# Optimization experiments

Measured on AMD Instinct MI355X. Metric: run time of the kernel, lower is better.

The kernel has to match this reference:

```python
import jax, jax.numpy as jnp
import numpy as np

IN_F = 4096
OUT_F = 4096
RANK = 8
ALPHA = 8
SCALE = ALPHA / RANK


def setup_inputs() -> dict:
    key = jax.random.key(0)
    kx, kw, kb, ka = jax.random.split(key, 4)
    x = jax.random.normal(kx, (4, 4096, IN_F), dtype=jnp.float32)
    # base frozen linear params (torch Linear default init style, any values ok)
    W = jax.random.normal(kw, (OUT_F, IN_F), dtype=jnp.float32) * (1.0 / np.sqrt(IN_F))
    b = jax.random.normal(kb, (OUT_F,), dtype=jnp.float32) * 0.01
    # lora_A: kaiming_uniform_(a=sqrt(5)) -> U(-bound, bound), bound = sqrt(6/((1+5)*in_f)) = 1/sqrt(in_f)
    bound = 1.0 / np.sqrt(IN_F)
    lora_A = jax.random.uniform(ka, (RANK, IN_F), dtype=jnp.float32, minval=-bound, maxval=bound)
    # lora_B initialized to zeros per module; use small random values so the LoRA path is exercised
    lora_B = jax.random.normal(jax.random.fold_in(key, 7), (OUT_F, RANK), dtype=jnp.float32) * 0.02
    return {"x": x, "W": W, "b": b, "lora_A": lora_A, "lora_B": lora_B}


def reference(x, W, b, lora_A, lora_B):
    # base: x @ W.T + b  [B,S,out_f]
    base = jnp.einsum("bsi,oi->bso", x, W) + b
    # low-rank path: (x @ A.T) @ B.T * scale
    xa = jnp.einsum("bsi,ri->bsr", x, lora_A)  # [B,S,r]
    lora = jnp.einsum("bsr,or->bso", xa, lora_B)
    return base + lora * SCALE
```

## Files before the change

### kernel.cpp

```cpp
#include <hip/hip_runtime.h>
#include <cstdint>

#define K_IN   4096
#define N_OUT  4096
#define M_ROWS 16384
#define RANK   8
#define LSCALE 1.0f
#define NT     64

typedef __attribute__((ext_vector_type(8))) short  short8;
typedef __attribute__((ext_vector_type(4))) float  floatx4;

__device__ __forceinline__ unsigned short f2bf(float f) {
  uint32_t u = __float_as_uint(f);
  u += 0x7FFFu + ((u >> 16) & 1u);
  return (unsigned short)(u >> 16);
}

__global__ __launch_bounds__(256) void fold_w_kernel(
    const float* __restrict__ W, const float* __restrict__ lA,
    const float* __restrict__ lB, unsigned short* __restrict__ Weff) {
  int idx = blockIdx.x * 256 + threadIdx.x;
  int o = idx >> 10;
  int k = (idx & 1023) << 2;
  float4 w = *reinterpret_cast<const float4*>(W + (size_t)o * K_IN + k);
#pragma unroll
  for (int r = 0; r < RANK; ++r) {
    float s = LSCALE * lB[o * RANK + r];
    float4 a = *reinterpret_cast<const float4*>(lA + r * K_IN + k);
    w.x += s * a.x; w.y += s * a.y; w.z += s * a.z; w.w += s * a.w;
  }
  ushort4 p;
  p.x = f2bf(w.x); p.y = f2bf(w.y); p.z = f2bf(w.z); p.w = f2bf(w.w);
  *reinterpret_cast<ushort4*>(Weff + (size_t)o * K_IN + k) = p;
}

__global__ __launch_bounds__(256) void cvt_x_kernel(
    const float* __restrict__ x, unsigned short* __restrict__ xb) {
  size_t i = ((size_t)blockIdx.x * 256 + threadIdx.x) * 8;
  float4 a = *reinterpret_cast<const float4*>(x + i);
  float4 c = *reinterpret_cast<const float4*>(x + i + 4);
  uint4 v;
  v.x = (uint32_t)f2bf(a.x) | ((uint32_t)f2bf(a.y) << 16);
  v.y = (uint32_t)f2bf(a.z) | ((uint32_t)f2bf(a.w) << 16);
  v.z = (uint32_t)f2bf(c.x) | ((uint32_t)f2bf(c.y) << 16);
  v.w = (uint32_t)f2bf(c.z) | ((uint32_t)f2bf(c.w) << 16);
  *reinterpret_cast<uint4*>(xb + i) = v;
}

__device__ __forceinline__ void gload_lds16(const void* g, void* l) {
  __builtin_amdgcn_global_load_lds(
      (const __attribute__((address_space(1))) void*)g,
      (__attribute__((address_space(3))) void*)l, 16, 0, 0);
}

__global__ __launch_bounds__(512, 2) void gemm_kernel(
    const unsigned short* __restrict__ Xb, const unsigned short* __restrict__ Wb,
    const float* __restrict__ bias, float* __restrict__ out) {
  __shared__ alignas(16) char lds[2 * 65536];

  const int tid  = threadIdx.x;
  const int wave = tid >> 6, lane = tid & 63;
  const int wr = wave >> 2, wc = wave & 3;
  const int l15 = lane & 15, sq = lane >> 4;
  const int xorv = (l15 & 7) << 4;

  int bx  = blockIdx.x;
  int sbx = (bx & 7) * 128 + (bx >> 3);
  const int mt = sbx >> 4;
  const int nt = sbx & 15;

  const unsigned short *gA0, *gA1, *gB0, *gB1;
  {
    int L0 = tid * 16;
    int r0 = ((L0 >> 7) << 1) | (((L0 >> 6) ^ (L0 >> 8)) & 1);
    int s0 = ((L0 >> 4) & 3) ^ (r0 & 3);
    gA0 = Xb + (size_t)(mt * 256 + r0) * K_IN + s0 * 8;
    gB0 = Wb + (size_t)(nt * 256 + r0) * K_IN + s0 * 8;
    int L1 = 8192 + tid * 16;
    int r1 = ((L1 >> 7) << 1) | (((L1 >> 6) ^ (L1 >> 8)) & 1);
    int s1 = ((L1 >> 4) & 3) ^ (r1 & 3);
    gA1 = Xb + (size_t)(mt * 256 + r1) * K_IN + s1 * 8;
    gB1 = Wb + (size_t)(nt * 256 + r1) * K_IN + s1 * 8;
  }

#define STAGE_A(TT, KS) do {                                         \
    char* d_ = lds + ((TT) & 1) * 65536 + (KS) * 16384 + tid * 16;   \
    gload_lds16(gA0 + (TT) * 64 + (KS) * 32, d_);                    \
    gload_lds16(gA1 + (TT) * 64 + (KS) * 32, d_ + 8192);             \
  } while (0)
#define STAGE_B(TT, KS) do {                                         \
    char* d_ = lds + ((TT) & 1) * 65536 + 32768 + (KS) * 16384 + tid * 16; \
    gload_lds16(gB0 + (TT) * 64 + (KS) * 32, d_);                    \
    gload_lds16(gB1 + (TT) * 64 + (KS) * 32, d_ + 8192);             \
  } while (0)
#define BAR() do { asm volatile("" ::: "memory");                    \
    __builtin_amdgcn_s_barrier();                                    \
    asm volatile("" ::: "memory"); } while (0)
#define LGKM0() asm volatile("s_waitcnt lgkmcnt(0)" ::: "memory")
#define LOAD_AF(MH, KS) do {                                         \
    const char* Ah_ = lds + tb + (KS) * 16384;                       \
    _Pragma("unroll")                                                \
    for (int i = 0; i < 4; ++i) {                                    \
      int rA_ = wr * 128 + ((MH) * 4 + i) * 16 + l15;                \
      int LA_ = ((rA_ << 6) | (sq << 4)) ^ xorv;                     \
      af[i] = *reinterpret_cast<const short8*>(Ah_ + LA_);           \
    } } while (0)
#define LOAD_BF(KS) do {                                             \
    const char* Bh_ = lds + tb + 32768 + (KS) * 16384;               \
    _Pragma("unroll")                                                \
    for (int j = 0; j < 4; ++j) {                                    \
      int rB_ = wc * 64 + j * 16 + l15;                              \
      int LB_ = ((rB_ << 6) | (sq << 4)) ^ xorv;                     \
      bf[j] = *reinterpret_cast<const short8*>(Bh_ + LB_);           \
    } } while (0)
#define DO_MFMA(MH) do {                                             \
    __builtin_amdgcn_s_setprio(1);                                   \
    _Pragma("unroll")                                                \
    for (int i = 0; i < 4; ++i)                                      \
      _Pragma("unroll")                                              \
      for (int j = 0; j < 4; ++j)                                    \
        acc[(MH) * 4 + i][j] = __builtin_amdgcn_mfma_f32_16x16x32_bf16( \
            af[i], bf[j], acc[(MH) * 4 + i][j], 0, 0, 0);            \
    __builtin_amdgcn_s_setprio(0); } while (0)

  floatx4 acc[8][4];
#pragma unroll
  for (int i = 0; i < 8; ++i)
#pragma unroll
    for (int j = 0; j < 4; ++j)
      acc[i][j] = (floatx4){0.f, 0.f, 0.f, 0.f};

  STAGE_A(0, 0); STAGE_B(0, 0); STAGE_A(0, 1); STAGE_B(0, 1);
  asm volatile("s_waitcnt vmcnt(4)" ::: "memory");
  BAR();

  short8 af[4], bf[4];

  for (int t = 0; t < NT; ++t) {
    const int tb = (t & 1) * 65536;
    const bool more = (t + 1 < NT);

    LOAD_AF(0, 0);
    LOAD_BF(0);
    if (more) STAGE_A(t + 1, 0);
    BAR(); LGKM0();
    DO_MFMA(0);
    BAR();

    LOAD_AF(1, 0);
    if (more) STAGE_B(t + 1, 0);
    BAR(); LGKM0();
    DO_MFMA(1);
    if (more) asm volatile("s_waitcnt vmcnt(4)" ::: "memory");
    else      asm volatile("s_waitcnt vmcnt(0)" ::: "memory");
    BAR();

    LOAD_AF(0, 1);
    LOAD_BF(1);
    if (more) STAGE_A(t + 1, 1);
    BAR(); LGKM0();
    DO_MFMA(0);
    BAR();

    LOAD_AF(1, 1);
    if (more) STAGE_B(t + 1, 1);
    BAR(); LGKM0();
    DO_MFMA(1);
    if (more) asm volatile("s_waitcnt vmcnt(4)" ::: "memory");
    BAR();
  }
#undef STAGE_A
#undef STAGE_B
#undef LOAD_AF
#undef LOAD_BF
#undef DO_MFMA

  const int row0 = mt * 256 + wr * 128 + sq * 4;
  const int col0 = nt * 256 + wc * 64 + l15;
#pragma unroll
  for (int j = 0; j < 4; ++j) {
    int col = col0 + j * 16;
    float bv = bias[col];
#pragma unroll
    for (int i = 0; i < 8; ++i) {
      int rowb = row0 + i * 16;
#pragma unroll
      for (int rr = 0; rr < 4; ++rr)
        out[(size_t)(rowb + rr) * N_OUT + col] = acc[i][j][rr] + bv;
    }
  }
}

__global__ __launch_bounds__(256) void fallback_kernel(
    const float* __restrict__ x, const float* __restrict__ W,
    const float* __restrict__ bias, const float* __restrict__ lA,
    const float* __restrict__ lB, float* __restrict__ out) {
  __shared__ float Xs[64][17];
  __shared__ float Ws[64][17];
  int tid = threadIdx.x;
  int tx = tid & 15, ty = tid >> 4;
  int bm = blockIdx.y * 64, bn = blockIdx.x * 64;
  float acc[4][4] = {};
  for (int k0 = 0; k0 < K_IN; k0 += 16) {
#pragma unroll
    for (int q = 0; q < 4; ++q) {
      int flat = q * 256 + tid;
      int r = flat >> 4, c = flat & 15;
      Xs[r][c] = x[(size_t)(bm + r) * K_IN + k0 + c];
      float w = W[(size_t)(bn + r) * K_IN + k0 + c];
#pragma unroll
      for (int rr = 0; rr < RANK; ++rr)
        w += LSCALE * lB[(bn + r) * RANK + rr] * lA[rr * K_IN + k0 + c];
      Ws[r][c] = w;
    }
    __syncthreads();
#pragma unroll
    for (int kk = 0; kk < 16; ++kk) {
      float av[4], bv[4];
#pragma unroll
      for (int i = 0; i < 4; ++i) av[i] = Xs[ty * 4 + i][kk];
#pragma unroll
      for (int j = 0; j < 4; ++j) bv[j] = Ws[tx * 4 + j][kk];
#pragma unroll
      for (int i = 0; i < 4; ++i)
#pragma unroll
        for (int j = 0; j < 4; ++j) acc[i][j] += av[i] * bv[j];
    }
    __syncthreads();
  }
#pragma unroll
  for (int i = 0; i < 4; ++i)
#pragma unroll
    for (int j = 0; j < 4; ++j)
      out[(size_t)(bm + ty * 4 + i) * N_OUT + bn + tx * 4 + j] =
          acc[i][j] + bias[bn + tx * 4 + j];
}

extern "C" void kernel_launch(void* const* d_in, const int* in_sizes, int n_in,
                              void* d_out, int out_size, void* d_ws, size_t ws_size,
                              hipStream_t stream) {
  const float* x  = (const float*)d_in[0];
  const float* W  = (const float*)d_in[1];
  const float* b  = (const float*)d_in[2];
  const float* lA = (const float*)d_in[3];
  const float* lB = (const float*)d_in[4];
  float* out = (float*)d_out;

  const size_t weff_bytes = (size_t)N_OUT * K_IN * 2;
  const size_t xb_bytes   = (size_t)M_ROWS * K_IN * 2;

  if (ws_size >= weff_bytes + xb_bytes) {
    unsigned short* Weff = (unsigned short*)d_ws;
    unsigned short* Xb   = (unsigned short*)((char*)d_ws + weff_bytes);
    fold_w_kernel<<<(int)(((size_t)N_OUT * K_IN / 4) / 256), 256, 0, stream>>>(W, lA, lB, Weff);
    cvt_x_kernel<<<(int)(((size_t)M_ROWS * K_IN / 8) / 256), 256, 0, stream>>>(x, Xb);
    gemm_kernel<<<(M_ROWS / 256) * (N_OUT / 256), 512, 0, stream>>>(Xb, Weff, b, out);
  } else {
    dim3 grid(N_OUT / 64, M_ROWS / 64);
    fallback_kernel<<<grid, 256, 0, stream>>>(x, W, b, lA, lB, out);
  }
}
```

Before: 638.9 us.

## Double-buffer LDS fragment registers to overlap ds_reads with MFMA

The main GEMM loop now loads the next set of A/B MFMA fragments from LDS into a second register set while the current set feeds the MFMAs, instead of waiting on lgkmcnt(0) before each MFMA group. The first fragment load of the next k-tile is hoisted into the tail of the current iteration, and the vmcnt waits are retuned to the new staging order. This aims to hide LDS read latency behind matrix math. In exchange it uses more VGPRs for fragments and relies on the compiler's implicit waits and on correct vmcnt accounting for cross-tile buffer reuse.

```diff
diff --git a/kernel.cpp b/kernel.cpp
--- a/kernel.cpp
+++ b/kernel.cpp
@@ -97,31 +97,30 @@
 #define BAR() do { asm volatile("" ::: "memory");                    \
     __builtin_amdgcn_s_barrier();                                    \
     asm volatile("" ::: "memory"); } while (0)
-#define LGKM0() asm volatile("s_waitcnt lgkmcnt(0)" ::: "memory")
-#define LOAD_AF(MH, KS) do {                                         \
-    const char* Ah_ = lds + tb + (KS) * 16384;                       \
+#define LOAD_AF(DST, BASE, MH, KS) do {                              \
+    const char* Ah_ = lds + (BASE) + (KS) * 16384;                   \
     _Pragma("unroll")                                                \
     for (int i = 0; i < 4; ++i) {                                    \
       int rA_ = wr * 128 + ((MH) * 4 + i) * 16 + l15;                \
       int LA_ = ((rA_ << 6) | (sq << 4)) ^ xorv;                     \
-      af[i] = *reinterpret_cast<const short8*>(Ah_ + LA_);           \
+      DST[i] = *reinterpret_cast<const short8*>(Ah_ + LA_);          \
     } } while (0)
-#define LOAD_BF(KS) do {                                             \
-    const char* Bh_ = lds + tb + 32768 + (KS) * 16384;               \
+#define LOAD_BF(DST, BASE, KS) do {                                  \
+    const char* Bh_ = lds + (BASE) + 32768 + (KS) * 16384;           \
     _Pragma("unroll")                                                \
     for (int j = 0; j < 4; ++j) {                                    \
       int rB_ = wc * 64 + j * 16 + l15;                              \
       int LB_ = ((rB_ << 6) | (sq << 4)) ^ xorv;                     \
-      bf[j] = *reinterpret_cast<const short8*>(Bh_ + LB_);           \
+      DST[j] = *reinterpret_cast<const short8*>(Bh_ + LB_);          \
     } } while (0)
-#define DO_MFMA(MH) do {                                             \
+#define DO_MFMA(MH, AF, BF) do {                                     \
     __builtin_amdgcn_s_setprio(1);                                   \
     _Pragma("unroll")                                                \
     for (int i = 0; i < 4; ++i)                                      \
       _Pragma("unroll")                                              \
       for (int j = 0; j < 4; ++j)                                    \
         acc[(MH) * 4 + i][j] = __builtin_amdgcn_mfma_f32_16x16x32_bf16( \
-            af[i], bf[j], acc[(MH) * 4 + i][j], 0, 0, 0);            \
+            AF[i], BF[j], acc[(MH) * 4 + i][j], 0, 0, 0);            \
     __builtin_amdgcn_s_setprio(0); } while (0)
 
   floatx4 acc[8][4];
@@ -135,39 +134,49 @@
   asm volatile("s_waitcnt vmcnt(4)" ::: "memory");
   BAR();
 
-  short8 af[4], bf[4];
+  short8 afA[4], afB[4], bfA[4], bfB[4];
+  LOAD_AF(afA, 0, 0, 0);
+  LOAD_BF(bfA, 0, 0);
 
   for (int t = 0; t < NT; ++t) {
     const int tb = (t & 1) * 65536;
+    const int nb = tb ^ 65536;
     const bool more = (t + 1 < NT);
 
-    LOAD_AF(0, 0);
-    LOAD_BF(0);
-    if (more) STAGE_A(t + 1, 0);
-    BAR(); LGKM0();
-    DO_MFMA(0);
-    BAR();
-
-    LOAD_AF(1, 0);
+    LOAD_AF(afB, tb, 1, 0);
+    if (more) {
+      STAGE_A(t + 1, 0);
+      asm volatile("s_waitcnt vmcnt(2)" ::: "memory");
+    } else {
+      asm volatile("s_waitcnt vmcnt(0)" ::: "memory");
+    }
+    BAR();
+    DO_MFMA(0, afA, bfA);
+    BAR();
+
+    LOAD_AF(afA, tb, 0, 1);
+    LOAD_BF(bfB, tb, 1);
     if (more) STAGE_B(t + 1, 0);
-    BAR(); LGKM0();
-    DO_MFMA(1);
-    if (more) asm volatile("s_waitcnt vmcnt(4)" ::: "memory");
-    else      asm volatile("s_waitcnt vmcnt(0)" ::: "memory");
-    BAR();
-
-    LOAD_AF(0, 1);
-    LOAD_BF(1);
-    if (more) STAGE_A(t + 1, 1);
-    BAR(); LGKM0();
-    DO_MFMA(0);
-    BAR();
-
-    LOAD_AF(1, 1);
-    if (more) STAGE_B(t + 1, 1);
-    BAR(); LGKM0();
-    DO_MFMA(1);
-    if (more) asm volatile("s_waitcnt vmcnt(4)" ::: "memory");
+    BAR();
+    DO_MFMA(1, afB, bfA);
+    BAR();
+
+    LOAD_AF(afB, tb, 1, 1);
+    if (more) {
+      STAGE_A(t + 1, 1);
+      asm volatile("s_waitcnt vmcnt(2)" ::: "memory");
+    }
+    BAR();
+    DO_MFMA(0, afA, bfB);
+    BAR();
+
+    if (more) {
+      LOAD_AF(afA, nb, 0, 0);
+      LOAD_BF(bfA, nb, 0);
+      STAGE_B(t + 1, 1);
+    }
+    BAR();
+    DO_MFMA(1, afB, bfB);
     BAR();
   }
 #undef STAGE_A
```

Result: slower. 691.2 us (+8.2%).
